# Optimization experiments

Hardware: AMD Instinct MI355X
Metric: run time of the kernel (lower is better)

The kernel has to match this reference:

```python
import jax, jax.numpy as jnp
import numpy as np

B, N, M, D, H = 2, 1024, 1024, 768, 72  # H = num_layers*nhead = 6*12

def setup_inputs() -> dict:
    key = jax.random.key(0)
    ks = jax.random.split(key, 7)
    s = lambda fan_in: 1.0 / np.sqrt(fan_in)
    return {
        "x": jax.random.normal(ks[0], (B, N, D), dtype=jnp.float32),
        "stacked_scores": jax.random.normal(ks[1], (B, H, N, M), dtype=jnp.float32),
        "W1": jax.random.uniform(ks[2], (D, D // 2), jnp.float32, -s(D), s(D)),
        "b1": jax.random.uniform(ks[3], (D // 2,), jnp.float32, -s(D), s(D)),
        "W2": jax.random.uniform(ks[4], (D // 2, H), jnp.float32, -s(D // 2), s(D // 2)),
        "b2": jax.random.uniform(ks[5], (H,), jnp.float32, -s(D // 2), s(D // 2)),
        "bias": jnp.zeros((1,), dtype=jnp.float32),
    }

def reference(x, stacked_scores, W1, b1, W2, b2, bias):
    # Router MLP: Linear -> exact GELU -> Linear  => raw_weights [b, n, h]
    h = jax.nn.gelu(jnp.einsum('bnd,df->bnf', x, W1) + b1, approximate=False)
    raw_weights = jnp.einsum('bnf,fh->bnh', h, W2) + b2
    # Weighted combine of stacked attention maps, reducing over heads
    final_matrix = jnp.einsum('bnh,bhnm->bnm', raw_weights, stacked_scores)
    return final_matrix + bias
```

## Files before the change

### kernel.cpp

```cpp
#include <hip/hip_runtime.h>
#include <math.h>

#define B_ 2
#define N_ 1024
#define M_ 1024
#define D_ 768
#define F_ 384
#define H_ 72

typedef float f32x4 __attribute__((ext_vector_type(4)));

__device__ float g_rw[B_ * N_ * H_];

__global__ __launch_bounds__(384) void mlp_kernel(
    const float* __restrict__ x, const float* __restrict__ W1,
    const float* __restrict__ b1, const float* __restrict__ W2,
    const float* __restrict__ b2)
{
    const int f = threadIdx.x;
    const int row0 = blockIdx.x * 8;

    __shared__ float xs[8][D_];
    __shared__ float hs[8][F_ + 8];

    {
        const f32x4* xg = reinterpret_cast<const f32x4*>(x + row0 * D_);
        f32x4* xl = reinterpret_cast<f32x4*>(&xs[0][0]);
#pragma unroll
        for (int i = 0; i < 4; ++i)
            xl[threadIdx.x + i * 384] = xg[threadIdx.x + i * 384];
    }
    __syncthreads();

    float acc[8];
#pragma unroll
    for (int r = 0; r < 8; ++r) acc[r] = 0.0f;

#pragma unroll 4
    for (int d = 0; d < D_; d += 4) {
        const float w0 = W1[(d + 0) * F_ + f];
        const float w1v = W1[(d + 1) * F_ + f];
        const float w2v = W1[(d + 2) * F_ + f];
        const float w3v = W1[(d + 3) * F_ + f];
#pragma unroll
        for (int r = 0; r < 8; ++r) {
            const float4 xv = *reinterpret_cast<const float4*>(&xs[r][d]);
            acc[r] = fmaf(xv.x, w0, acc[r]);
            acc[r] = fmaf(xv.y, w1v, acc[r]);
            acc[r] = fmaf(xv.z, w2v, acc[r]);
            acc[r] = fmaf(xv.w, w3v, acc[r]);
        }
    }

    const float bb = b1[f];
#pragma unroll
    for (int r = 0; r < 8; ++r) {
        const float v = acc[r] + bb;
        hs[r][f] = 0.5f * v * (1.0f + erff(v * 0.70710678118654752f));
    }
    __syncthreads();

#pragma unroll 1
    for (int o = f; o < 8 * H_; o += 384) {
        const int r = o / H_;
        const int c = o - r * H_;
        float s = 0.0f;
#pragma unroll 4
        for (int k = 0; k < F_; k += 4) {
            const float4 hv = *reinterpret_cast<const float4*>(&hs[r][k]);
            s = fmaf(hv.x, W2[(k + 0) * H_ + c], s);
            s = fmaf(hv.y, W2[(k + 1) * H_ + c], s);
            s = fmaf(hv.z, W2[(k + 2) * H_ + c], s);
            s = fmaf(hv.w, W2[(k + 3) * H_ + c], s);
        }
        g_rw[row0 * H_ + o] = s + b2[c];
    }
}

__global__ __launch_bounds__(256) void combine_kernel(
    const float* __restrict__ scores, const float* __restrict__ bias,
    float* __restrict__ out)
{
    const int blk = blockIdx.x;
    const int b = blk >> 8;
    const int n0 = (blk & 255) * 4;
    const int t = threadIdx.x;

    __shared__ float w[4 * H_];
    for (int i = t; i < 4 * H_; i += 256)
        w[i] = g_rw[((b << 10) + n0) * H_ + i];
    __syncthreads();

    const f32x4* __restrict__ sp = reinterpret_cast<const f32x4*>(scores);
    const int base = ((b * H_) * N_ + n0) * (M_ / 4) + t;
    const int hstr = N_ * (M_ / 4);

    f32x4 a0 = 0.f, a1 = 0.f, a2 = 0.f, a3 = 0.f;
#pragma unroll 2
    for (int h = 0; h < H_; ++h) {
        const int ib = base + h * hstr;
        const f32x4 v0 = __builtin_nontemporal_load(sp + ib);
        const f32x4 v1 = __builtin_nontemporal_load(sp + ib + 256);
        const f32x4 v2 = __builtin_nontemporal_load(sp + ib + 512);
        const f32x4 v3 = __builtin_nontemporal_load(sp + ib + 768);
        const float w0 = w[0 * H_ + h];
        const float w1 = w[1 * H_ + h];
        const float w2 = w[2 * H_ + h];
        const float w3 = w[3 * H_ + h];
#pragma unroll
        for (int j = 0; j < 4; ++j) {
            a0[j] = fmaf(w0, v0[j], a0[j]);
            a1[j] = fmaf(w1, v1[j], a1[j]);
            a2[j] = fmaf(w2, v2[j], a2[j]);
            a3[j] = fmaf(w3, v3[j], a3[j]);
        }
    }

    const float bv = bias[0];
    f32x4* __restrict__ op = reinterpret_cast<f32x4*>(out);
    const int obase = ((b << 10) + n0) * (M_ / 4) + t;
#pragma unroll
    for (int j = 0; j < 4; ++j) { a0[j] += bv; a1[j] += bv; a2[j] += bv; a3[j] += bv; }
    __builtin_nontemporal_store(a0, op + obase);
    __builtin_nontemporal_store(a1, op + obase + 256);
    __builtin_nontemporal_store(a2, op + obase + 512);
    __builtin_nontemporal_store(a3, op + obase + 768);
}

extern "C" void kernel_launch(void* const* d_in, const int* in_sizes, int n_in,
                              void* d_out, int out_size, void* d_ws, size_t ws_size,
                              hipStream_t stream) {
    const float* x      = (const float*)d_in[0];
    const float* scores = (const float*)d_in[1];
    const float* W1     = (const float*)d_in[2];
    const float* b1     = (const float*)d_in[3];
    const float* W2     = (const float*)d_in[4];
    const float* b2     = (const float*)d_in[5];
    const float* bias   = (const float*)d_in[6];
    float* out = (float*)d_out;

    mlp_kernel<<<(B_ * N_) / 8, 384, 0, stream>>>(x, W1, b1, W2, b2);
    combine_kernel<<<(B_ * N_) / 4, 256, 0, stream>>>(scores, bias, out);
}
```

Before: 143.9 us.

## Fuse router MLP and score combine into a single kernel

```diff
diff --git a/kernel.cpp b/kernel.cpp
--- a/kernel.cpp
+++ b/kernel.cpp
@@ -7,61 +7,67 @@
 #define D_ 768
 #define F_ 384
 #define H_ 72
+#define ROWS 8
 
 typedef float f32x4 __attribute__((ext_vector_type(4)));
 
-__device__ float g_rw[B_ * N_ * H_];
+__global__ __launch_bounds__(512) void fused_kernel(
+    const float* __restrict__ x, const float* __restrict__ scores,
+    const float* __restrict__ W1, const float* __restrict__ b1,
+    const float* __restrict__ W2, const float* __restrict__ b2,
+    const float* __restrict__ bias, float* __restrict__ out)
+{
+    const int t = threadIdx.x;
+    const int blk = blockIdx.x;
+    const int b = blk >> 7;
+    const int n0 = (blk & 127) * ROWS;
+    const int row0 = (b << 10) + n0;
 
-__global__ __launch_bounds__(384) void mlp_kernel(
-    const float* __restrict__ x, const float* __restrict__ W1,
-    const float* __restrict__ b1, const float* __restrict__ W2,
-    const float* __restrict__ b2)
-{
-    const int f = threadIdx.x;
-    const int row0 = blockIdx.x * 8;
-
-    __shared__ float xs[8][D_];
-    __shared__ float hs[8][F_ + 8];
+    __shared__ float xs[ROWS][D_];
+    __shared__ float hs[ROWS][F_ + 8];
+    __shared__ float rw[ROWS][80];
 
     {
         const f32x4* xg = reinterpret_cast<const f32x4*>(x + row0 * D_);
         f32x4* xl = reinterpret_cast<f32x4*>(&xs[0][0]);
 #pragma unroll
-        for (int i = 0; i < 4; ++i)
-            xl[threadIdx.x + i * 384] = xg[threadIdx.x + i * 384];
+        for (int i = 0; i < 3; ++i)
+            xl[t + i * 512] = xg[t + i * 512];
     }
     __syncthreads();
 
-    float acc[8];
+    if (t < F_) {
+        const int f = t;
+        float acc[ROWS];
 #pragma unroll
-    for (int r = 0; r < 8; ++r) acc[r] = 0.0f;
+        for (int r = 0; r < ROWS; ++r) acc[r] = 0.0f;
 
 #pragma unroll 4
-    for (int d = 0; d < D_; d += 4) {
-        const float w0 = W1[(d + 0) * F_ + f];
-        const float w1v = W1[(d + 1) * F_ + f];
-        const float w2v = W1[(d + 2) * F_ + f];
-        const float w3v = W1[(d + 3) * F_ + f];
+        for (int d = 0; d < D_; d += 4) {
+            const float w0 = W1[(d + 0) * F_ + f];
+            const float w1v = W1[(d + 1) * F_ + f];
+            const float w2v = W1[(d + 2) * F_ + f];
+            const float w3v = W1[(d + 3) * F_ + f];
 #pragma unroll
-        for (int r = 0; r < 8; ++r) {
-            const float4 xv = *reinterpret_cast<const float4*>(&xs[r][d]);
-            acc[r] = fmaf(xv.x, w0, acc[r]);
-            acc[r] = fmaf(xv.y, w1v, acc[r]);
-            acc[r] = fmaf(xv.z, w2v, acc[r]);
-            acc[r] = fmaf(xv.w, w3v, acc[r]);
+            for (int r = 0; r < ROWS; ++r) {
+                const float4 xv = *reinterpret_cast<const float4*>(&xs[r][d]);
+                acc[r] = fmaf(xv.x, w0, acc[r]);
+                acc[r] = fmaf(xv.y, w1v, acc[r]);
+                acc[r] = fmaf(xv.z, w2v, acc[r]);
+                acc[r] = fmaf(xv.w, w3v, acc[r]);
+            }
         }
-    }
-
-    const float bb = b1[f];
+        const float bb = b1[f];
 #pragma unroll
-    for (int r = 0; r < 8; ++r) {
-        const float v = acc[r] + bb;
-        hs[r][f] = 0.5f * v * (1.0f + erff(v * 0.70710678118654752f));
+        for (int r = 0; r < ROWS; ++r) {
+            const float v = acc[r] + bb;
+            hs[r][f] = 0.5f * v * (1.0f + erff(v * 0.70710678118654752f));
+        }
     }
     __syncthreads();
 
 #pragma unroll 1
-    for (int o = f; o < 8 * H_; o += 384) {
+    for (int o = t; o < ROWS * H_; o += 512) {
         const int r = o / H_;
         const int c = o - r * H_;
         float s = 0.0f;
@@ -73,26 +79,16 @@
             s = fmaf(hv.z, W2[(k + 2) * H_ + c], s);
             s = fmaf(hv.w, W2[(k + 3) * H_ + c], s);
         }
-        g_rw[row0 * H_ + o] = s + b2[c];
+        rw[r][c] = s + b2[c];
     }
-}
-
-__global__ __launch_bounds__(256) void combine_kernel(
-    const float* __restrict__ scores, const float* __restrict__ bias,
-    float* __restrict__ out)
-{
-    const int blk = blockIdx.x;
-    const int b = blk >> 8;
-    const int n0 = (blk & 255) * 4;
-    const int t = threadIdx.x;
-
-    __shared__ float w[4 * H_];
-    for (int i = t; i < 4 * H_; i += 256)
-        w[i] = g_rw[((b << 10) + n0) * H_ + i];
     __syncthreads();
 
+    const int col = t & 255;
+    const int rp = t >> 8;
+    const int r0 = rp * 4;
+
     const f32x4* __restrict__ sp = reinterpret_cast<const f32x4*>(scores);
-    const int base = ((b * H_) * N_ + n0) * (M_ / 4) + t;
+    const int base = ((b * H_) * N_ + (n0 + r0)) * (M_ / 4) + col;
     const int hstr = N_ * (M_ / 4);
 
     f32x4 a0 = 0.f, a1 = 0.f, a2 = 0.f, a3 = 0.f;
@@ -103,10 +99,10 @@
         const f32x4 v1 = __builtin_nontemporal_load(sp + ib + 256);
         const f32x4 v2 = __builtin_nontemporal_load(sp + ib + 512);
         const f32x4 v3 = __builtin_nontemporal_load(sp + ib + 768);
-        const float w0 = w[0 * H_ + h];
-        const float w1 = w[1 * H_ + h];
-        const float w2 = w[2 * H_ + h];
-        const float w3 = w[3 * H_ + h];
+        const float w0 = rw[r0 + 0][h];
+        const float w1 = rw[r0 + 1][h];
+        const float w2 = rw[r0 + 2][h];
+        const float w3 = rw[r0 + 3][h];
 #pragma unroll
         for (int j = 0; j < 4; ++j) {
             a0[j] = fmaf(w0, v0[j], a0[j]);
@@ -117,10 +113,11 @@
     }
 
     const float bv = bias[0];
-    f32x4* __restrict__ op = reinterpret_cast<f32x4*>(out);
-    const int obase = ((b << 10) + n0) * (M_ / 4) + t;
 #pragma unroll
     for (int j = 0; j < 4; ++j) { a0[j] += bv; a1[j] += bv; a2[j] += bv; a3[j] += bv; }
+
+    f32x4* __restrict__ op = reinterpret_cast<f32x4*>(out);
+    const int obase = (row0 + r0) * (M_ / 4) + col;
     __builtin_nontemporal_store(a0, op + obase);
     __builtin_nontemporal_store(a1, op + obase + 256);
     __builtin_nontemporal_store(a2, op + obase + 512);
@@ -139,6 +136,6 @@
     const float* bias   = (const float*)d_in[6];
     float* out = (float*)d_out;
 
-    mlp_kernel<<<(B_ * N_) / 8, 384, 0, stream>>>(x, W1, b1, W2, b2);
-    combine_kernel<<<(B_ * N_) / 4, 256, 0, stream>>>(scores, bias, out);
+    fused_kernel<<<(B_ * N_) / ROWS, 512, 0, stream>>>(
+        x, scores, W1, b1, W2, b2, bias, out);
 }
```

After: 146.0 us. Within noise of the previous version (+1.5%).
